# Kernel tuning notes

Hardware: AMD Instinct MI355X
Metric: run time of the kernel (lower is better)

Reference implementation:

```python
import jax, jax.numpy as jnp
import numpy as np

N = 100000      # nodes
E = 3200000     # edges (avg degree 32)
F_IN = 16       # node_feature_size
R1, R2, R3 = 8, 16, 8   # gcn hidden sizes
N1 = 32                  # mlp hidden


def _lin(k, fan_in, shape):
    s = 1.0 / np.sqrt(fan_in)
    return jax.random.uniform(k, shape, minval=-s, maxval=s, dtype=jnp.float32)


def setup_inputs() -> dict:
    key = jax.random.key(0)
    ks = jax.random.split(key, 16)
    x = jax.random.normal(ks[0], (N, F_IN), dtype=jnp.float32)
    edge_index = jax.random.randint(ks[1], (2, E), 0, N, dtype=jnp.int64)
    return {
        "x": x,
        "edge_index": edge_index,
        # GraphConv k: out = mean_agg(x_j) @ W_rel + b + x @ W_root  (PyG GraphConv, lin_root bias=False)
        "W_rel1": _lin(ks[2], F_IN, (F_IN, R1)), "b1": _lin(ks[3], F_IN, (R1,)), "W_root1": _lin(ks[4], F_IN, (F_IN, R1)),
        "W_rel2": _lin(ks[5], R1, (R1, R2)),   "b2": _lin(ks[6], R1, (R2,)),   "W_root2": _lin(ks[7], R1, (R1, R2)),
        "W_rel3": _lin(ks[8], R2, (R2, R3)),   "b3": _lin(ks[9], R2, (R3,)),   "W_root3": _lin(ks[10], R2, (R2, R3)),
        "fc1_W": _lin(ks[11], R3, (R3, N1)), "fc1_b": _lin(ks[12], R3, (N1,)),
        "fc2_W": _lin(ks[13], N1, (N1, 1)),  "fc2_b": _lin(ks[14], N1, (1,)),
    }


def _graph_conv(x, src, dst, W_rel, b, W_root):
    # message: gather source features; aggregate: mean over incoming edges at dst
    n = x.shape[0]
    msg_sum = jax.ops.segment_sum(x[src], dst, num_segments=n)          # [N, F]
    cnt = jax.ops.segment_sum(jnp.ones(src.shape, x.dtype), dst, num_segments=n)
    mean = msg_sum / jnp.maximum(cnt, 1.0)[:, None]
    return mean @ W_rel + b + x @ W_root


def reference(x, edge_index, W_rel1, b1, W_root1, W_rel2, b2, W_root2,
              W_rel3, b3, W_root3, fc1_W, fc1_b, fc2_W, fc2_b):
    src, dst = edge_index[0], edge_index[1]
    h = jax.nn.sigmoid(_graph_conv(x, src, dst, W_rel1, b1, W_root1))
    h = jax.nn.sigmoid(_graph_conv(h, src, dst, W_rel2, b2, W_root2))
    h = jax.nn.sigmoid(_graph_conv(h, src, dst, W_rel3, b3, W_root3))
    h = jax.nn.sigmoid(h @ fc1_W + fc1_b)
    return h @ fc2_W + fc2_b   # [N, 1]
```

## Files before the change

### kernel.cpp

```cpp
#include <hip/hip_runtime.h>
#include <math.h>


#define CHUNK 4096
#define BW    128
#define MAXB  6144
#define MAXNB 1024
#define MAXBLK 1024

typedef _Float16 half8 __attribute__((ext_vector_type(8)));
typedef _Float16 half4 __attribute__((ext_vector_type(4)));

static __device__ __forceinline__ float sigmoidf_(float x) {
    return 1.0f / (1.0f + expf(-x));
}

static __device__ __forceinline__ int scan256_excl(int v, int* s) {
    int tid = threadIdx.x;
    s[tid] = v;
    for (int off = 1; off < 256; off <<= 1) {
        __syncthreads();
        int t = (tid >= off) ? s[tid - off] : 0;
        __syncthreads();
        s[tid] += t;
    }
    __syncthreads();
    return s[tid] - v;
}

__global__ __launch_bounds__(256)
void x_half_kernel(const float* __restrict__ x, _Float16* __restrict__ xh, int n4) {
    int i = blockIdx.x * 256 + threadIdx.x;
    if (i < n4) {
        const float4* x4 = (const float4*)x;
        float4 v = x4[i];
        half4 h = {(_Float16)v.x, (_Float16)v.y, (_Float16)v.z, (_Float16)v.w};
        ((half4*)xh)[i] = h;
    }
}

__global__ __launch_bounds__(256)
void bin_sort_kernel(const int* __restrict__ src, const int* __restrict__ dst,
                     unsigned* __restrict__ packed, int* __restrict__ counts_bm,
                     int* __restrict__ lstart_bm, int E, int NB) {
    __shared__ int s_hist[MAXNB];
    __shared__ int s_cur[MAXNB];
    __shared__ unsigned s_pk[CHUNK];
    __shared__ int s_scan[256];
    int tid = threadIdx.x, blk = blockIdx.x;
    for (int i = tid; i < NB; i += 256) s_hist[i] = 0;
    __syncthreads();

    int base = blk * CHUNK;
    int cnt = E - base; if (cnt > CHUNK) cnt = CHUNK;

    unsigned pk[16]; int bk[16]; int nk = 0;
    if (cnt == CHUNK) {
        const int4* s4 = (const int4*)(src + base);
        const int4* d4 = (const int4*)(dst + base);
#pragma unroll
        for (int k = 0; k < 4; ++k) {
            int4 s = s4[tid * 4 + k];
            int4 d = d4[tid * 4 + k];
            int ds[4] = {d.x, d.y, d.z, d.w};
            int ss[4] = {s.x, s.y, s.z, s.w};
#pragma unroll
            for (int j = 0; j < 4; ++j) {
                int b = ds[j] >> 7;
                bk[nk] = b;
                pk[nk] = ((unsigned)(ds[j] & 127) << 17) | (unsigned)ss[j];
                atomicAdd(&s_hist[b], 1);
                ++nk;
            }
        }
    } else {
        for (int i = tid; i < cnt; i += 256) {
            int d = dst[base + i], s = src[base + i];
            int b = d >> 7;
            bk[nk] = b;
            pk[nk] = ((unsigned)(d & 127) << 17) | (unsigned)s;
            atomicAdd(&s_hist[b], 1);
            ++nk;
        }
    }
    __syncthreads();

    int per = (NB + 255) / 256;
    int st = tid * per;
    int lsum = 0;
    for (int j = 0; j < per; ++j)
        if (st + j < NB) lsum += s_hist[st + j];
    int excl = scan256_excl(lsum, s_scan);
    int run = excl;
    for (int j = 0; j < per; ++j)
        if (st + j < NB) { s_cur[st + j] = run; run += s_hist[st + j]; }
    __syncthreads();

    for (int k = 0; k < nk; ++k) {
        int pos = atomicAdd(&s_cur[bk[k]], 1);
        s_pk[pos] = pk[k];
    }
    __syncthreads();

    for (int i = tid; i < cnt; i += 256) packed[base + i] = s_pk[i];
    for (int i = tid; i < NB; i += 256) {
        int h = s_hist[i];
        counts_bm[blk * NB + i] = h;
        lstart_bm[blk * NB + i] = s_cur[i] - h;
    }
}

__global__ __launch_bounds__(256)
void transpose2_kernel(const int* __restrict__ a, int* __restrict__ at,
                       const int* __restrict__ b, int* __restrict__ bt,
                       int rows, int cols) {
    __shared__ int ta[32][33];
    __shared__ int tb[32][33];
    int tx = threadIdx.x & 31, ty = threadIdx.x >> 5;
    int r0 = blockIdx.y * 32, c0 = blockIdx.x * 32;
#pragma unroll
    for (int k = 0; k < 4; ++k) {
        int r = r0 + ty + 8 * k, c = c0 + tx;
        if (r < rows && c < cols) {
            ta[ty + 8 * k][tx] = a[r * cols + c];
            tb[ty + 8 * k][tx] = b[r * cols + c];
        }
    }
    __syncthreads();
#pragma unroll
    for (int k = 0; k < 4; ++k) {
        int c = c0 + ty + 8 * k, r = r0 + tx;
        if (c < cols && r < rows) {
            at[c * rows + r] = ta[tx][ty + 8 * k];
            bt[c * rows + r] = tb[tx][ty + 8 * k];
        }
    }
}

__global__ __launch_bounds__(256)
void btot_kernel(const int* __restrict__ counts_t, int* __restrict__ btot, int NBLK) {
    __shared__ int s_scan[256];
    int b = blockIdx.x, tid = threadIdx.x;
    int v = 0;
    for (int i = tid; i < NBLK; i += 256) v += counts_t[b * NBLK + i];
    scan256_excl(v, s_scan);
    if (tid == 255) btot[b] = s_scan[255];
}

__global__ __launch_bounds__(1024)
void bscan_kernel(const int* __restrict__ btot, int* __restrict__ bstart, int NB) {
    __shared__ int lds[1024];
    int tid = threadIdx.x;
    int v = (tid < NB) ? btot[tid] : 0;
    lds[tid] = v;
    for (int off = 1; off < 1024; off <<= 1) {
        __syncthreads();
        int t = (tid >= off) ? lds[tid - off] : 0;
        __syncthreads();
        lds[tid] += t;
    }
    __syncthreads();
    if (tid < NB) bstart[tid] = lds[tid] - v;
}

__global__ __launch_bounds__(256)
void bucket_sort_kernel(const unsigned* __restrict__ packed,
                        const int* __restrict__ counts_t,
                        const int* __restrict__ lstart_t,
                        const int* __restrict__ bstart,
                        int* __restrict__ csr_src, int* __restrict__ deg,
                        int* __restrict__ rowstart, int N, int NB, int NBLK) {
    __shared__ int s_cnt[MAXBLK], s_lst[MAXBLK], s_off[MAXBLK];
    __shared__ unsigned s_p[MAXB];
    __shared__ int s_out[MAXB];
    __shared__ int h[BW], hs[BW], curb[BW];
    __shared__ int s_scan[256];
    __shared__ int s_tot;
    int b = blockIdx.x, tid = threadIdx.x;
    int beg = bstart[b];

    for (int i = tid; i < NBLK; i += 256) {
        s_cnt[i] = counts_t[b * NBLK + i];
        s_lst[i] = lstart_t[b * NBLK + i];
    }
    __syncthreads();

    int per = (NBLK + 255) / 256;
    int st = tid * per;
    int lsum = 0;
    for (int j = 0; j < per; ++j)
        if (st + j < NBLK) lsum += s_cnt[st + j];
    int excl = scan256_excl(lsum, s_scan);
    if (tid == 255) s_tot = s_scan[255];
    int run = excl;
    for (int j = 0; j < per; ++j)
        if (st + j < NBLK) { s_off[st + j] = run; run += s_cnt[st + j]; }
    __syncthreads();
    int cnt = s_tot; if (cnt > MAXB) cnt = MAXB;

    for (int blk = tid; blk < NBLK; blk += 256) {
        int c = s_cnt[blk], o = s_off[blk];
        const unsigned* p = packed + (size_t)blk * CHUNK + s_lst[blk];
        for (int j = 0; j < c; ++j) s_p[o + j] = p[j];
    }
    if (tid < BW) h[tid] = 0;
    __syncthreads();

    for (int i = tid; i < cnt; i += 256) atomicAdd(&h[s_p[i] >> 17], 1);
    __syncthreads();
    if (tid == 0) {
        int acc = 0;
        for (int i = 0; i < BW; ++i) { hs[i] = acc; acc += h[i]; }
    }
    __syncthreads();
    if (tid < BW) {
        curb[tid] = hs[tid];
        int node = b * BW + tid;
        if (node < N) { deg[node] = h[tid]; rowstart[node] = beg + hs[tid]; }
    }
    __syncthreads();
    for (int i = tid; i < cnt; i += 256) {
        unsigned p = s_p[i];
        int pos = atomicAdd(&curb[p >> 17], 1);
        s_out[pos] = (int)(p & 0x1FFFF);
    }
    __syncthreads();
    for (int i = tid; i < cnt; i += 256) csr_src[beg + i] = s_out[i];
}

template <int FIN, int FOUT>
__global__ __launch_bounds__(256)
void gcn_layer_kernel(const _Float16* __restrict__ hin,
                      const int* __restrict__ rowstart,
                      const int* __restrict__ deg,
                      const int* __restrict__ csr_src,
                      const float* __restrict__ Wrel,
                      const float* __restrict__ bias,
                      const float* __restrict__ Wroot,
                      _Float16* __restrict__ hout, int n) {
    constexpr int LPN = FIN / 8;
    constexpr int NPB = 256 / LPN;
    __shared__ float s_mean[NPB * FIN];
    __shared__ float s_x[NPB * FIN];
    __shared__ float s_Wrel[FIN * FOUT];
    __shared__ float s_Wroot[FIN * FOUT];
    __shared__ float s_b[FOUT];

    int tid = threadIdx.x;
    for (int i = tid; i < FIN * FOUT; i += 256) {
        s_Wrel[i] = Wrel[i];
        s_Wroot[i] = Wroot[i];
    }
    if (tid < FOUT) s_b[tid] = bias[tid];

    int ln = tid / LPN, q = tid % LPN;
    int node = blockIdx.x * NPB + ln;
    const half8* hin8 = (const half8*)hin;

    if (node < n) {
        half8 selfv = hin8[node * LPN + q];
        int rs = rowstart[node];
        int d = deg[node];
        float s[8] = {0, 0, 0, 0, 0, 0, 0, 0};
        int e = 0;
        for (; e + 2 <= d; e += 2) {
            int s0 = csr_src[rs + e];
            int s1 = csr_src[rs + e + 1];
            half8 v0 = hin8[s0 * LPN + q];
            half8 v1 = hin8[s1 * LPN + q];
#pragma unroll
            for (int c = 0; c < 8; ++c) s[c] += (float)v0[c] + (float)v1[c];
        }
        if (e < d) {
            half8 v0 = hin8[csr_src[rs + e] * LPN + q];
#pragma unroll
            for (int c = 0; c < 8; ++c) s[c] += (float)v0[c];
        }
        float inv = 1.0f / (float)(d > 0 ? d : 1);
        int base = ln * FIN + q * 8;
#pragma unroll
        for (int c = 0; c < 8; ++c) {
            s_mean[base + c] = s[c] * inv;
            s_x[base + c] = (float)selfv[c];
        }
    }
    __syncthreads();

    for (int o = tid; o < NPB * FOUT; o += 256) {
        int l = o / FOUT, j = o % FOUT;
        int nd = blockIdx.x * NPB + l;
        if (nd < n) {
            float acc = s_b[j];
#pragma unroll
            for (int ff = 0; ff < FIN; ++ff)
                acc += s_mean[l * FIN + ff] * s_Wrel[ff * FOUT + j]
                     + s_x[l * FIN + ff]    * s_Wroot[ff * FOUT + j];
            hout[nd * FOUT + j] = (_Float16)sigmoidf_(acc);
        }
    }
}

__global__ __launch_bounds__(256)
void mlp_kernel(const _Float16* __restrict__ h3,
                const float* __restrict__ fc1W, const float* __restrict__ fc1b,
                const float* __restrict__ fc2W, const float* __restrict__ fc2b,
                float* __restrict__ out, int n) {
    __shared__ float s_W1[8 * 32];
    __shared__ float s_b1[32];
    __shared__ float s_W2[32];
    __shared__ float s_b2;
    int tid = threadIdx.x;
    if (tid < 256) s_W1[tid] = fc1W[tid];
    if (tid < 32) { s_b1[tid] = fc1b[tid]; s_W2[tid] = fc2W[tid]; }
    if (tid == 0) s_b2 = fc2b[0];
    __syncthreads();

    int node = blockIdx.x * 256 + tid;
    if (node < n) {
        half8 a = ((const half8*)h3)[node];
        float h[8];
#pragma unroll
        for (int f = 0; f < 8; ++f) h[f] = (float)a[f];
        float acc = s_b2;
#pragma unroll
        for (int j = 0; j < 32; ++j) {
            float v = s_b1[j];
#pragma unroll
            for (int f = 0; f < 8; ++f) v += h[f] * s_W1[f * 32 + j];
            acc += s_W2[j] * sigmoidf_(v);
        }
        out[node] = acc;
    }
}

extern "C" void kernel_launch(void* const* d_in, const int* in_sizes, int n_in,
                              void* d_out, int out_size, void* d_ws, size_t ws_size,
                              hipStream_t stream) {
    const float* x      = (const float*)d_in[0];
    const int*   ei     = (const int*)d_in[1];
    const float* Wrel1  = (const float*)d_in[2];
    const float* b1     = (const float*)d_in[3];
    const float* Wroot1 = (const float*)d_in[4];
    const float* Wrel2  = (const float*)d_in[5];
    const float* b2     = (const float*)d_in[6];
    const float* Wroot2 = (const float*)d_in[7];
    const float* Wrel3  = (const float*)d_in[8];
    const float* b3     = (const float*)d_in[9];
    const float* Wroot3 = (const float*)d_in[10];
    const float* fc1W   = (const float*)d_in[11];
    const float* fc1b   = (const float*)d_in[12];
    const float* fc2W   = (const float*)d_in[13];
    const float* fc2b   = (const float*)d_in[14];
    float* out = (float*)d_out;

    const int N = in_sizes[0] / 16;
    const int E = in_sizes[1] / 2;
    const int* e_src = ei;
    const int* e_dst = ei + E;

    const int NB   = (N + BW - 1) / BW;
    const int NBLK = (E + CHUNK - 1) / CHUNK;

    char* ws = (char*)d_ws;
    size_t off = 0;
    auto alloc = [&](size_t bytes) { char* p = ws + off; off += (bytes + 15) & ~size_t(15); return p; };
    unsigned* packed   = (unsigned*)alloc((size_t)NBLK * CHUNK * 4);
    int* counts_bm     = (int*)alloc((size_t)NBLK * NB * 4);
    int* lstart_bm     = (int*)alloc((size_t)NBLK * NB * 4);
    int* counts_t      = (int*)alloc((size_t)NBLK * NB * 4);
    int* lstart_t      = (int*)alloc((size_t)NBLK * NB * 4);
    int* btot          = (int*)alloc((size_t)NB * 4);
    int* bstart        = (int*)alloc((size_t)NB * 4);
    int* csr_src       = (int*)alloc((size_t)E * 4);
    int* deg           = (int*)alloc((size_t)N * 4);
    int* rowstart      = (int*)alloc((size_t)N * 4);
    _Float16* xh       = (_Float16*)alloc((size_t)N * 16 * 2);
    _Float16* h1       = (_Float16*)alloc((size_t)N * 8 * 2);
    _Float16* h2       = (_Float16*)alloc((size_t)N * 16 * 2);
    _Float16* h3       = (_Float16*)alloc((size_t)N * 8 * 2);

    bin_sort_kernel<<<NBLK, 256, 0, stream>>>(e_src, e_dst, packed, counts_bm, lstart_bm, E, NB);
    dim3 tgrid((NB + 31) / 32, (NBLK + 31) / 32);
    transpose2_kernel<<<tgrid, 256, 0, stream>>>(counts_bm, counts_t, lstart_bm, lstart_t, NBLK, NB);
    btot_kernel<<<NB, 256, 0, stream>>>(counts_t, btot, NBLK);
    bscan_kernel<<<1, 1024, 0, stream>>>(btot, bstart, NB);
    bucket_sort_kernel<<<NB, 256, 0, stream>>>(packed, counts_t, lstart_t, bstart,
                                               csr_src, deg, rowstart, N, NB, NBLK);

    x_half_kernel<<<(N * 4 + 255) / 256, 256, 0, stream>>>(x, xh, N * 4);
    gcn_layer_kernel<16, 8><<<(N + 127) / 128, 256, 0, stream>>>(
        xh, rowstart, deg, csr_src, Wrel1, b1, Wroot1, h1, N);
    gcn_layer_kernel<8, 16><<<(N + 255) / 256, 256, 0, stream>>>(
        h1, rowstart, deg, csr_src, Wrel2, b2, Wroot2, h2, N);
    gcn_layer_kernel<16, 8><<<(N + 127) / 128, 256, 0, stream>>>(
        h2, rowstart, deg, csr_src, Wrel3, b3, Wroot3, h3, N);
    mlp_kernel<<<(N + 255) / 256, 256, 0, stream>>>(
        h3, fc1W, fc1b, fc2W, fc2b, out, N);
}
```

Before: 268.3 us.

## Transform features before aggregation, fuse GCN layers, and pad CSR rows

Uses linearity of mean aggregation to apply the relation and root weights before gathering. Layers 1 and 3 now gather 8-wide fp16 rows instead of 16-wide ones. Layer 2's output transform is fused with layer 3's pre-transform, and layer 3's aggregation with the MLP, which drops the separate x-to-half and MLP kernels. CSR rows are padded to multiples of 4 so neighbor indices can be read with int4 loads. The bin sort now takes larger chunks and reads edges twice instead of holding them in registers. The trade-offs are extra fp16 rounding of transformed features, a larger CSR buffer, and uninitialized padding slots that the degree bounds must keep from being read.

```diff
diff --git a/kernel.cpp b/kernel.cpp
--- a/kernel.cpp
+++ b/kernel.cpp
@@ -2,14 +2,13 @@
 #include <math.h>
 
 
-#define CHUNK 4096
-#define BW    128
-#define MAXB  6144
-#define MAXNB 1024
-#define MAXBLK 1024
+#define CHUNK  8192
+#define BW     128
+#define MAXB   6144
+#define MAXNB  800
+#define MAXBLK 512
 
 typedef _Float16 half8 __attribute__((ext_vector_type(8)));
-typedef _Float16 half4 __attribute__((ext_vector_type(4)));
 
 static __device__ __forceinline__ float sigmoidf_(float x) {
     return 1.0f / (1.0f + expf(-x));
@@ -28,15 +27,65 @@
     return s[tid] - v;
 }
 
-__global__ __launch_bounds__(256)
-void x_half_kernel(const float* __restrict__ x, _Float16* __restrict__ xh, int n4) {
-    int i = blockIdx.x * 256 + threadIdx.x;
-    if (i < n4) {
-        const float4* x4 = (const float4*)x;
-        float4 v = x4[i];
-        half4 h = {(_Float16)v.x, (_Float16)v.y, (_Float16)v.z, (_Float16)v.w};
-        ((half4*)xh)[i] = h;
-    }
+static __device__ __forceinline__ void gather_mean8(
+    const half8* __restrict__ t, const int* __restrict__ csr,
+    int rs, int d, float* s) {
+#pragma unroll
+    for (int c = 0; c < 8; ++c) s[c] = 0.0f;
+    int e = 0;
+    for (; e + 4 <= d; e += 4) {
+        int4 ci = *(const int4*)(csr + rs + e);
+        half8 v0 = t[ci.x]; half8 v1 = t[ci.y];
+        half8 v2 = t[ci.z]; half8 v3 = t[ci.w];
+#pragma unroll
+        for (int c = 0; c < 8; ++c)
+            s[c] += ((float)v0[c] + (float)v1[c]) + ((float)v2[c] + (float)v3[c]);
+    }
+    for (; e < d; ++e) {
+        half8 v = t[csr[rs + e]];
+#pragma unroll
+        for (int c = 0; c < 8; ++c) s[c] += (float)v[c];
+    }
+    float inv = 1.0f / (float)(d > 0 ? d : 1);
+#pragma unroll
+    for (int c = 0; c < 8; ++c) s[c] *= inv;
+}
+
+__global__ __launch_bounds__(256)
+void transform1_kernel(const float* __restrict__ x, const float* __restrict__ Wrel,
+                       const float* __restrict__ bias, const float* __restrict__ Wroot,
+                       _Float16* __restrict__ t1, _Float16* __restrict__ z1, int n) {
+    __shared__ float sWr[128], sWo[128], sb[8];
+    int tid = threadIdx.x;
+    if (tid < 128) { sWr[tid] = Wrel[tid]; sWo[tid] = Wroot[tid]; }
+    if (tid < 8) sb[tid] = bias[tid];
+    __syncthreads();
+    int node = blockIdx.x * 256 + tid;
+    if (node >= n) return;
+    const float4* x4 = (const float4*)x;
+    float xv[16];
+#pragma unroll
+    for (int k = 0; k < 4; ++k) {
+        float4 v = x4[node * 4 + k];
+        xv[4 * k] = v.x; xv[4 * k + 1] = v.y; xv[4 * k + 2] = v.z; xv[4 * k + 3] = v.w;
+    }
+    float ta[8], za[8];
+#pragma unroll
+    for (int j = 0; j < 8; ++j) { ta[j] = 0.0f; za[j] = sb[j]; }
+#pragma unroll
+    for (int f = 0; f < 16; ++f) {
+        float xf = xv[f];
+#pragma unroll
+        for (int j = 0; j < 8; ++j) {
+            ta[j] += xf * sWr[f * 8 + j];
+            za[j] += xf * sWo[f * 8 + j];
+        }
+    }
+    half8 th, zh;
+#pragma unroll
+    for (int j = 0; j < 8; ++j) { th[j] = (_Float16)ta[j]; zh[j] = (_Float16)za[j]; }
+    ((half8*)t1)[node] = th;
+    ((half8*)z1)[node] = zh;
 }
 
 __global__ __launch_bounds__(256)
@@ -54,34 +103,18 @@
     int base = blk * CHUNK;
     int cnt = E - base; if (cnt > CHUNK) cnt = CHUNK;
 
-    unsigned pk[16]; int bk[16]; int nk = 0;
     if (cnt == CHUNK) {
-        const int4* s4 = (const int4*)(src + base);
         const int4* d4 = (const int4*)(dst + base);
 #pragma unroll
-        for (int k = 0; k < 4; ++k) {
-            int4 s = s4[tid * 4 + k];
-            int4 d = d4[tid * 4 + k];
-            int ds[4] = {d.x, d.y, d.z, d.w};
-            int ss[4] = {s.x, s.y, s.z, s.w};
-#pragma unroll
-            for (int j = 0; j < 4; ++j) {
-                int b = ds[j] >> 7;
-                bk[nk] = b;
-                pk[nk] = ((unsigned)(ds[j] & 127) << 17) | (unsigned)ss[j];
-                atomicAdd(&s_hist[b], 1);
-                ++nk;
-            }
+        for (int k = 0; k < CHUNK / 1024; ++k) {
+            int4 d = d4[k * 256 + tid];
+            atomicAdd(&s_hist[d.x >> 7], 1);
+            atomicAdd(&s_hist[d.y >> 7], 1);
+            atomicAdd(&s_hist[d.z >> 7], 1);
+            atomicAdd(&s_hist[d.w >> 7], 1);
         }
     } else {
-        for (int i = tid; i < cnt; i += 256) {
-            int d = dst[base + i], s = src[base + i];
-            int b = d >> 7;
-            bk[nk] = b;
-            pk[nk] = ((unsigned)(d & 127) << 17) | (unsigned)s;
-            atomicAdd(&s_hist[b], 1);
-            ++nk;
-        }
+        for (int i = tid; i < cnt; i += 256) atomicAdd(&s_hist[dst[base + i] >> 7], 1);
     }
     __syncthreads();
 
@@ -96,9 +129,27 @@
         if (st + j < NB) { s_cur[st + j] = run; run += s_hist[st + j]; }
     __syncthreads();
 
-    for (int k = 0; k < nk; ++k) {
-        int pos = atomicAdd(&s_cur[bk[k]], 1);
-        s_pk[pos] = pk[k];
+    if (cnt == CHUNK) {
+        const int4* d4 = (const int4*)(dst + base);
+        const int4* s4 = (const int4*)(src + base);
+#pragma unroll
+        for (int k = 0; k < CHUNK / 1024; ++k) {
+            int4 d = d4[k * 256 + tid];
+            int4 s = s4[k * 256 + tid];
+            int dd[4] = {d.x, d.y, d.z, d.w};
+            int ss[4] = {s.x, s.y, s.z, s.w};
+#pragma unroll
+            for (int j = 0; j < 4; ++j) {
+                int pos = atomicAdd(&s_cur[dd[j] >> 7], 1);
+                s_pk[pos] = ((unsigned)(dd[j] & 127) << 17) | (unsigned)ss[j];
+            }
+        }
+    } else {
+        for (int i = tid; i < cnt; i += 256) {
+            int d = dst[base + i], s = src[base + i];
+            int pos = atomicAdd(&s_cur[d >> 7], 1);
+            s_pk[pos] = ((unsigned)(d & 127) << 17) | (unsigned)s;
+        }
     }
     __syncthreads();
 
@@ -151,7 +202,7 @@
 void bscan_kernel(const int* __restrict__ btot, int* __restrict__ bstart, int NB) {
     __shared__ int lds[1024];
     int tid = threadIdx.x;
-    int v = (tid < NB) ? btot[tid] : 0;
+    int v = (tid < NB) ? (((btot[tid] + 3) & ~3) + 512) : 0;
     lds[tid] = v;
     for (int off = 1; off < 1024; off <<= 1) {
         __syncthreads();
@@ -175,7 +226,7 @@
     __shared__ int s_out[MAXB];
     __shared__ int h[BW], hs[BW], curb[BW];
     __shared__ int s_scan[256];
-    __shared__ int s_tot;
+    __shared__ int s_tot, s_ptot;
     int b = blockIdx.x, tid = threadIdx.x;
     int beg = bstart[b];
 
@@ -210,7 +261,8 @@
     __syncthreads();
     if (tid == 0) {
         int acc = 0;
-        for (int i = 0; i < BW; ++i) { hs[i] = acc; acc += h[i]; }
+        for (int i = 0; i < BW; ++i) { hs[i] = acc; acc += (h[i] + 3) & ~3; }
+        s_ptot = acc;
     }
     __syncthreads();
     if (tid < BW) {
@@ -225,112 +277,114 @@
         s_out[pos] = (int)(p & 0x1FFFF);
     }
     __syncthreads();
-    for (int i = tid; i < cnt; i += 256) csr_src[beg + i] = s_out[i];
-}
-
-template <int FIN, int FOUT>
-__global__ __launch_bounds__(256)
-void gcn_layer_kernel(const _Float16* __restrict__ hin,
-                      const int* __restrict__ rowstart,
-                      const int* __restrict__ deg,
-                      const int* __restrict__ csr_src,
-                      const float* __restrict__ Wrel,
-                      const float* __restrict__ bias,
-                      const float* __restrict__ Wroot,
-                      _Float16* __restrict__ hout, int n) {
-    constexpr int LPN = FIN / 8;
-    constexpr int NPB = 256 / LPN;
-    __shared__ float s_mean[NPB * FIN];
-    __shared__ float s_x[NPB * FIN];
-    __shared__ float s_Wrel[FIN * FOUT];
-    __shared__ float s_Wroot[FIN * FOUT];
-    __shared__ float s_b[FOUT];
-
+    int ptot = s_ptot; if (ptot > MAXB) ptot = MAXB;
+    for (int i = tid; i < ptot; i += 256) csr_src[beg + i] = s_out[i];
+}
+
+__global__ __launch_bounds__(256)
+void agg1_kernel(const _Float16* __restrict__ t1, const _Float16* __restrict__ z1,
+                 const int* __restrict__ rowstart, const int* __restrict__ deg,
+                 const int* __restrict__ csr, _Float16* __restrict__ h1, int n) {
+    int node = blockIdx.x * 256 + threadIdx.x;
+    if (node >= n) return;
+    float s[8];
+    gather_mean8((const half8*)t1, csr, rowstart[node], deg[node], s);
+    half8 z = ((const half8*)z1)[node];
+    half8 o;
+#pragma unroll
+    for (int c = 0; c < 8; ++c) o[c] = (_Float16)sigmoidf_(s[c] + (float)z[c]);
+    ((half8*)h1)[node] = o;
+}
+
+__global__ __launch_bounds__(256)
+void gcn2_fused_kernel(const _Float16* __restrict__ h1,
+                       const int* __restrict__ rowstart, const int* __restrict__ deg,
+                       const int* __restrict__ csr,
+                       const float* __restrict__ W2r, const float* __restrict__ b2,
+                       const float* __restrict__ W2o,
+                       const float* __restrict__ W3r, const float* __restrict__ b3,
+                       const float* __restrict__ W3o,
+                       _Float16* __restrict__ t3, _Float16* __restrict__ z3, int n) {
+    __shared__ float sW2r[128], sW2o[128], sW3r[128], sW3o[128], sb2[16], sb3[8];
     int tid = threadIdx.x;
-    for (int i = tid; i < FIN * FOUT; i += 256) {
-        s_Wrel[i] = Wrel[i];
-        s_Wroot[i] = Wroot[i];
-    }
-    if (tid < FOUT) s_b[tid] = bias[tid];
-
-    int ln = tid / LPN, q = tid % LPN;
-    int node = blockIdx.x * NPB + ln;
-    const half8* hin8 = (const half8*)hin;
-
-    if (node < n) {
-        half8 selfv = hin8[node * LPN + q];
-        int rs = rowstart[node];
-        int d = deg[node];
-        float s[8] = {0, 0, 0, 0, 0, 0, 0, 0};
-        int e = 0;
-        for (; e + 2 <= d; e += 2) {
-            int s0 = csr_src[rs + e];
-            int s1 = csr_src[rs + e + 1];
-            half8 v0 = hin8[s0 * LPN + q];
-            half8 v1 = hin8[s1 * LPN + q];
-#pragma unroll
-            for (int c = 0; c < 8; ++c) s[c] += (float)v0[c] + (float)v1[c];
-        }
-        if (e < d) {
-            half8 v0 = hin8[csr_src[rs + e] * LPN + q];
-#pragma unroll
-            for (int c = 0; c < 8; ++c) s[c] += (float)v0[c];
-        }
-        float inv = 1.0f / (float)(d > 0 ? d : 1);
-        int base = ln * FIN + q * 8;
-#pragma unroll
-        for (int c = 0; c < 8; ++c) {
-            s_mean[base + c] = s[c] * inv;
-            s_x[base + c] = (float)selfv[c];
-        }
-    }
-    __syncthreads();
-
-    for (int o = tid; o < NPB * FOUT; o += 256) {
-        int l = o / FOUT, j = o % FOUT;
-        int nd = blockIdx.x * NPB + l;
-        if (nd < n) {
-            float acc = s_b[j];
-#pragma unroll
-            for (int ff = 0; ff < FIN; ++ff)
-                acc += s_mean[l * FIN + ff] * s_Wrel[ff * FOUT + j]
-                     + s_x[l * FIN + ff]    * s_Wroot[ff * FOUT + j];
-            hout[nd * FOUT + j] = (_Float16)sigmoidf_(acc);
-        }
-    }
-}
-
-__global__ __launch_bounds__(256)
-void mlp_kernel(const _Float16* __restrict__ h3,
-                const float* __restrict__ fc1W, const float* __restrict__ fc1b,
-                const float* __restrict__ fc2W, const float* __restrict__ fc2b,
-                float* __restrict__ out, int n) {
-    __shared__ float s_W1[8 * 32];
-    __shared__ float s_b1[32];
-    __shared__ float s_W2[32];
-    __shared__ float s_b2;
+    if (tid < 128) {
+        sW2r[tid] = W2r[tid]; sW2o[tid] = W2o[tid];
+        sW3r[tid] = W3r[tid]; sW3o[tid] = W3o[tid];
+    }
+    if (tid < 16) sb2[tid] = b2[tid];
+    if (tid < 8) sb3[tid] = b3[tid];
+    __syncthreads();
+    int node = blockIdx.x * 256 + tid;
+    if (node >= n) return;
+
+    float m[8];
+    gather_mean8((const half8*)h1, csr, rowstart[node], deg[node], m);
+    half8 sf = ((const half8*)h1)[node];
+    float x8[8];
+#pragma unroll
+    for (int c = 0; c < 8; ++c) x8[c] = (float)sf[c];
+
+    float v16[16];
+#pragma unroll
+    for (int j = 0; j < 16; ++j) {
+        float a = sb2[j];
+#pragma unroll
+        for (int f = 0; f < 8; ++f)
+            a += m[f] * sW2r[f * 16 + j] + x8[f] * sW2o[f * 16 + j];
+        v16[j] = sigmoidf_(a);
+    }
+    float ta[8], za[8];
+#pragma unroll
+    for (int j = 0; j < 8; ++j) { ta[j] = 0.0f; za[j] = sb3[j]; }
+#pragma unroll
+    for (int f = 0; f < 16; ++f) {
+        float hv = v16[f];
+#pragma unroll
+        for (int j = 0; j < 8; ++j) {
+            ta[j] += hv * sW3r[f * 8 + j];
+            za[j] += hv * sW3o[f * 8 + j];
+        }
+    }
+    half8 th, zh;
+#pragma unroll
+    for (int j = 0; j < 8; ++j) { th[j] = (_Float16)ta[j]; zh[j] = (_Float16)za[j]; }
+    ((half8*)t3)[node] = th;
+    ((half8*)z3)[node] = zh;
+}
+
+__global__ __launch_bounds__(256)
+void agg3_mlp_kernel(const _Float16* __restrict__ t3, const _Float16* __restrict__ z3,
+                     const int* __restrict__ rowstart, const int* __restrict__ deg,
+                     const int* __restrict__ csr,
+                     const float* __restrict__ fc1W, const float* __restrict__ fc1b,
+                     const float* __restrict__ fc2W, const float* __restrict__ fc2b,
+                     float* __restrict__ out, int n) {
+    __shared__ float sW1[256], sb1[32], sW2[32];
+    __shared__ float sb2_;
     int tid = threadIdx.x;
-    if (tid < 256) s_W1[tid] = fc1W[tid];
-    if (tid < 32) { s_b1[tid] = fc1b[tid]; s_W2[tid] = fc2W[tid]; }
-    if (tid == 0) s_b2 = fc2b[0];
-    __syncthreads();
-
+    if (tid < 256) sW1[tid] = fc1W[tid];
+    if (tid < 32) { sb1[tid] = fc1b[tid]; sW2[tid] = fc2W[tid]; }
+    if (tid == 0) sb2_ = fc2b[0];
+    __syncthreads();
     int node = blockIdx.x * 256 + tid;
-    if (node < n) {
-        half8 a = ((const half8*)h3)[node];
-        float h[8];
-#pragma unroll
-        for (int f = 0; f < 8; ++f) h[f] = (float)a[f];
-        float acc = s_b2;
-#pragma unroll
-        for (int j = 0; j < 32; ++j) {
-            float v = s_b1[j];
-#pragma unroll
-            for (int f = 0; f < 8; ++f) v += h[f] * s_W1[f * 32 + j];
-            acc += s_W2[j] * sigmoidf_(v);
-        }
-        out[node] = acc;
-    }
+    if (node >= n) return;
+
+    float s[8];
+    gather_mean8((const half8*)t3, csr, rowstart[node], deg[node], s);
+    half8 z = ((const half8*)z3)[node];
+    float h[8];
+#pragma unroll
+    for (int c = 0; c < 8; ++c) h[c] = sigmoidf_(s[c] + (float)z[c]);
+
+    float acc = sb2_;
+#pragma unroll
+    for (int j = 0; j < 32; ++j) {
+        float a = sb1[j];
+#pragma unroll
+        for (int f = 0; f < 8; ++f) a += h[f] * sW1[f * 32 + j];
+        acc += sW2[j] * sigmoidf_(a);
+    }
+    out[node] = acc;
 }
 
 extern "C" void kernel_launch(void* const* d_in, const int* in_sizes, int n_in,
@@ -371,13 +425,18 @@
     int* lstart_t      = (int*)alloc((size_t)NBLK * NB * 4);
     int* btot          = (int*)alloc((size_t)NB * 4);
     int* bstart        = (int*)alloc((size_t)NB * 4);
-    int* csr_src       = (int*)alloc((size_t)E * 4);
+    int* csr_src       = (int*)alloc(((size_t)E + (size_t)NB * 516) * 4);
     int* deg           = (int*)alloc((size_t)N * 4);
     int* rowstart      = (int*)alloc((size_t)N * 4);
-    _Float16* xh       = (_Float16*)alloc((size_t)N * 16 * 2);
+    _Float16* t1       = (_Float16*)alloc((size_t)N * 8 * 2);
+    _Float16* z1       = (_Float16*)alloc((size_t)N * 8 * 2);
     _Float16* h1       = (_Float16*)alloc((size_t)N * 8 * 2);
-    _Float16* h2       = (_Float16*)alloc((size_t)N * 16 * 2);
-    _Float16* h3       = (_Float16*)alloc((size_t)N * 8 * 2);
+    _Float16* t3       = (_Float16*)alloc((size_t)N * 8 * 2);
+    _Float16* z3       = (_Float16*)alloc((size_t)N * 8 * 2);
+
+    const int nbN = (N + 255) / 256;
+
+    transform1_kernel<<<nbN, 256, 0, stream>>>(x, Wrel1, b1, Wroot1, t1, z1, N);
 
     bin_sort_kernel<<<NBLK, 256, 0, stream>>>(e_src, e_dst, packed, counts_bm, lstart_bm, E, NB);
     dim3 tgrid((NB + 31) / 32, (NBLK + 31) / 32);
@@ -387,13 +446,9 @@
     bucket_sort_kernel<<<NB, 256, 0, stream>>>(packed, counts_t, lstart_t, bstart,
                                                csr_src, deg, rowstart, N, NB, NBLK);
 
-    x_half_kernel<<<(N * 4 + 255) / 256, 256, 0, stream>>>(x, xh, N * 4);
-    gcn_layer_kernel<16, 8><<<(N + 127) / 128, 256, 0, stream>>>(
-        xh, rowstart, deg, csr_src, Wrel1, b1, Wroot1, h1, N);
-    gcn_layer_kernel<8, 16><<<(N + 255) / 256, 256, 0, stream>>>(
-        h1, rowstart, deg, csr_src, Wrel2, b2, Wroot2, h2, N);
-    gcn_layer_kernel<16, 8><<<(N + 127) / 128, 256, 0, stream>>>(
-        h2, rowstart, deg, csr_src, Wrel3, b3, Wroot3, h3, N);
-    mlp_kernel<<<(N + 255) / 256, 256, 0, stream>>>(
-        h3, fc1W, fc1b, fc2W, fc2b, out, N);
-}
+    agg1_kernel<<<nbN, 256, 0, stream>>>(t1, z1, rowstart, deg, csr_src, h1, N);
+    gcn2_fused_kernel<<<nbN, 256, 0, stream>>>(h1, rowstart, deg, csr_src,
+                                               Wrel2, b2, Wroot2, Wrel3, b3, Wroot3, t3, z3, N);
+    agg3_mlp_kernel<<<nbN, 256, 0, stream>>>(t3, z3, rowstart, deg, csr_src,
+                                             fc1W, fc1b, fc2W, fc2b, out, N);
+}
```

New measurement: 232.0 us. -13.5%, faster.
